# Optimization experiments

Hardware: AMD Instinct MI355X
Metric: run time of the kernel (lower is better)

## Reference

```python
import jax, jax.numpy as jnp
import numpy as np

NUM_HIDDEN = 128
NUM_IN = 256
NUM_HEADS = 4
B, T, N, K = 4, 32, 96, 30


def setup_inputs() -> dict:
    key = jax.random.key(0)
    ks = jax.random.split(key, 7)
    return {
        "h_V": jax.random.normal(ks[0], (B, T, N, NUM_HIDDEN), dtype=jnp.float32),
        "h_EV": jax.random.normal(ks[1], (B, T, N, K, NUM_IN), dtype=jnp.float32),
        "mask_attend": jax.random.randint(ks[2], (B, T, N, K), 0, 2, dtype=jnp.int32),
        "Wq": jax.random.normal(ks[3], (NUM_HIDDEN, NUM_HIDDEN), dtype=jnp.float32) / np.sqrt(NUM_HIDDEN),
        "Wk": jax.random.normal(ks[4], (NUM_IN, NUM_HIDDEN), dtype=jnp.float32) / np.sqrt(NUM_IN),
        "Wv": jax.random.normal(ks[5], (NUM_IN, NUM_HIDDEN), dtype=jnp.float32) / np.sqrt(NUM_IN),
        "Wo": jax.random.normal(ks[6], (NUM_HIDDEN, NUM_HIDDEN), dtype=jnp.float32) / np.sqrt(NUM_HIDDEN),
    }


def reference(h_V, h_EV, mask_attend, Wq, Wk, Wv, Wo):
    b, t, n, k = h_EV.shape[:4]
    h = NUM_HEADS
    d = NUM_HIDDEN // h
    # projections
    Q = (h_V @ Wq).reshape(b, t, n, h, d)            # [B,T,N,H,d]
    Kp = (h_EV @ Wk).reshape(b, t, n, k, h, d)       # [B,T,N,K,H,d]
    V = (h_EV @ Wv).reshape(b, t, n, k, h, d)        # [B,T,N,K,H,d]
    # per-node neighbor attention logits [B,T,N,H,K]
    logits = jnp.einsum('btnhd,btnkhd->btnhk', Q, Kp) / jnp.sqrt(jnp.float32(d))
    neg_inf = jnp.finfo(jnp.float32).min
    mask = mask_attend[:, :, :, None, :]             # [B,T,N,1,K] -> broadcast over heads
    logits = jnp.where(mask > 0, logits, neg_inf)
    attend = jax.nn.softmax(logits, axis=-1)
    attend = attend * mask.astype(jnp.float32)
    # combine values: [B,T,N,H,d]
    out = jnp.einsum('btnhk,btnkhd->btnhd', attend, V).reshape(b, t, n, NUM_HIDDEN)
    return out @ Wo
```

## Files before the change

kernel.cpp:

```cpp
#include <hip/hip_runtime.h>
#include <hip/hip_bf16.h>
#include <cfloat>
#include <math.h>

constexpr int SITES = 12288;
constexpr int KNB   = 30;
constexpr int CIN   = 256;
#define RSQRT_D 0.17677669529663689f

typedef short bf16x8 __attribute__((ext_vector_type(8)));
typedef float f32x4  __attribute__((ext_vector_type(4)));

__device__ inline unsigned short f2bs(float x) {
    __hip_bfloat16 b = __float2bfloat16(x);
    return *(unsigned short*)&b;
}
__device__ inline float bs2f(unsigned short u) {
    unsigned int v = (unsigned int)u << 16;
    float f;
    __builtin_memcpy(&f, &v, 4);
    return f;
}
__device__ inline unsigned int pack2(float a, float b) {
    return (unsigned int)f2bs(a) | ((unsigned int)f2bs(b) << 16);
}

__global__ __launch_bounds__(256) void precompute_w(
    const float* __restrict__ Wq, const float* __restrict__ Wk,
    const float* __restrict__ Wv, const float* __restrict__ Wo,
    unsigned short* __restrict__ Mt, unsigned short* __restrict__ W3t) {
    int gid = blockIdx.x * 256 + threadIdx.x;
    if (gid < 131072) {
        int p = gid >> 7;
        int i = gid & 127;
        int h = p >> 8;
        int c = p & 255;
        float s = 0.f;
        #pragma unroll
        for (int d = 0; d < 32; ++d)
            s += Wq[i * 128 + h * 32 + d] * Wk[c * 128 + h * 32 + d];
        Mt[gid] = f2bs(s);
    } else {
        int o = gid - 131072;
        int j = o >> 10;
        int rest = o & 1023;
        int h = rest >> 8;
        int c = rest & 255;
        float s = 0.f;
        #pragma unroll
        for (int d = 0; d < 32; ++d)
            s += Wv[c * 128 + h * 32 + d] * Wo[(h * 32 + d) * 128 + j];
        W3t[o] = f2bs(s);
    }
}

__global__ __launch_bounds__(256) void convert_hv(
    const float* __restrict__ hV, unsigned short* __restrict__ hVb) {
    int gid = blockIdx.x * 256 + threadIdx.x;
    const float4* src = (const float4*)hV;
    float4 a = src[gid * 2];
    float4 b = src[gid * 2 + 1];
    uint4 p;
    p.x = pack2(a.x, a.y);
    p.y = pack2(a.z, a.w);
    p.z = pack2(b.x, b.y);
    p.w = pack2(b.z, b.w);
    ((uint4*)hVb)[gid] = p;
}

template <bool OUT_BF16>
__global__ __launch_bounds__(256) void gemm_bt_bf16(
    const unsigned short* __restrict__ A, const unsigned short* __restrict__ Bt,
    void* __restrict__ C, int M, int N, int K) {
    constexpr int BM = 64, BN = 128, BK = 32, PAD = 8;
    constexpr int NT = BN / 16;
    __shared__ unsigned short As[BM][BK + PAD];
    __shared__ unsigned short Bs[BN][BK + PAD];
    const int tid  = threadIdx.x;
    const int wave = tid >> 6;
    const int lane = tid & 63;
    const int quad = lane >> 4;
    const int l16  = lane & 15;
    const int bm0 = blockIdx.x * BM;
    const int bn0 = blockIdx.y * BN;

    f32x4 acc[NT];
    #pragma unroll
    for (int j = 0; j < NT; ++j) acc[j] = (f32x4){0.f, 0.f, 0.f, 0.f};

    for (int kk = 0; kk < K; kk += BK) {
        {
            int row = tid >> 2, off = (tid & 3) * 8;
            *(uint4*)&As[row][off] =
                *(const uint4*)&A[(size_t)(bm0 + row) * K + kk + off];
        }
        #pragma unroll
        for (int i = 0; i < 2; ++i) {
            int c = tid * 2 + i;
            int row = c >> 2, off = (c & 3) * 8;
            *(uint4*)&Bs[row][off] =
                *(const uint4*)&Bt[(size_t)(bn0 + row) * K + kk + off];
        }
        __syncthreads();
        bf16x8 af = *(const bf16x8*)&As[wave * 16 + l16][quad * 8];
        #pragma unroll
        for (int j = 0; j < NT; ++j) {
            bf16x8 bf = *(const bf16x8*)&Bs[j * 16 + l16][quad * 8];
            acc[j] = __builtin_amdgcn_mfma_f32_16x16x32_bf16(af, bf, acc[j], 0, 0, 0);
        }
        __syncthreads();
    }
    int row0 = bm0 + wave * 16 + quad * 4;
    #pragma unroll
    for (int j = 0; j < NT; ++j) {
        int col = bn0 + j * 16 + l16;
        #pragma unroll
        for (int r = 0; r < 4; ++r) {
            if (OUT_BF16)
                ((unsigned short*)C)[(size_t)(row0 + r) * N + col] = f2bs(acc[j][r]);
            else
                ((float*)C)[(size_t)(row0 + r) * N + col] = acc[j][r];
        }
    }
}

__global__ __launch_bounds__(256) void attn_kernel(
    const float* __restrict__ hEV, const int* __restrict__ mask,
    const unsigned short* __restrict__ qt, unsigned short* __restrict__ evb) {
    __shared__ unsigned short evS[KNB * CIN];
    __shared__ float logitsL[4 * 32];
    __shared__ float attendL[4 * 32];
    __shared__ int   activeS[32];
    __shared__ int   naS;

    const int s = blockIdx.x;
    const int tid = threadIdx.x;
    const int lane = tid & 63;
    const int sub = tid & 15;

    if (tid < 64) {
        int mk = (tid < KNB) ? mask[(size_t)s * KNB + tid] : 0;
        unsigned long long bal = __ballot(mk > 0);
        if (tid == 0) naS = __popcll(bal);
        if (mk > 0) activeS[__popcll(bal & ((1ull << tid) - 1))] = tid;
    }

    float qf[4][16];
    {
        const uint4* q4 = (const uint4*)(qt + (size_t)s * 1024);
        #pragma unroll
        for (int h = 0; h < 4; ++h) {
            #pragma unroll
            for (int c = 0; c < 2; ++c) {
                uint4 u = q4[h * 32 + sub * 2 + c];
                qf[h][c * 8 + 0] = bs2f(u.x & 0xffff);
                qf[h][c * 8 + 1] = bs2f(u.x >> 16);
                qf[h][c * 8 + 2] = bs2f(u.y & 0xffff);
                qf[h][c * 8 + 3] = bs2f(u.y >> 16);
                qf[h][c * 8 + 4] = bs2f(u.z & 0xffff);
                qf[h][c * 8 + 5] = bs2f(u.z >> 16);
                qf[h][c * 8 + 6] = bs2f(u.w & 0xffff);
                qf[h][c * 8 + 7] = bs2f(u.w >> 16);
            }
        }
    }
    __syncthreads();
    const int na = naS;

    for (int r = tid >> 4; r < na; r += 16) {
        int k = activeS[r];
        const float4* row4 = (const float4*)(hEV + (size_t)s * (KNB * CIN) + (size_t)k * CIN);
        float vv[16];
        #pragma unroll
        for (int i = 0; i < 4; ++i)
            *(float4*)&vv[i * 4] = row4[sub * 4 + i];

        uint4 p0, p1;
        p0.x = pack2(vv[0], vv[1]);  p0.y = pack2(vv[2], vv[3]);
        p0.z = pack2(vv[4], vv[5]);  p0.w = pack2(vv[6], vv[7]);
        p1.x = pack2(vv[8], vv[9]);  p1.y = pack2(vv[10], vv[11]);
        p1.z = pack2(vv[12], vv[13]); p1.w = pack2(vv[14], vv[15]);
        *(uint4*)&evS[r * CIN + sub * 16]     = p0;
        *(uint4*)&evS[r * CIN + sub * 16 + 8] = p1;

        float l[4] = {0.f, 0.f, 0.f, 0.f};
        #pragma unroll
        for (int h = 0; h < 4; ++h)
            #pragma unroll
            for (int c = 0; c < 16; ++c)
                l[h] = fmaf(vv[c], qf[h][c], l[h]);

        #pragma unroll
        for (int m = 1; m < 16; m <<= 1) {
            #pragma unroll
            for (int h = 0; h < 4; ++h) l[h] += __shfl_xor(l[h], m, 64);
        }
        if (sub == 0) {
            #pragma unroll
            for (int h = 0; h < 4; ++h) logitsL[h * 32 + r] = l[h] * RSQRT_D;
        }
    }
    __syncthreads();

    {
        int h = tid >> 6;
        float lg = (lane < na) ? logitsL[h * 32 + lane] : -FLT_MAX;
        float mx = lg;
        #pragma unroll
        for (int m = 1; m < 64; m <<= 1) mx = fmaxf(mx, __shfl_xor(mx, m, 64));
        float e = (lane < na) ? __expf(lg - mx) : 0.f;
        float sm = e;
        #pragma unroll
        for (int m = 1; m < 64; m <<= 1) sm += __shfl_xor(sm, m, 64);
        if (lane < na) attendL[h * 32 + lane] = e / sm;
    }
    __syncthreads();

    float a0 = 0.f, a1 = 0.f, a2 = 0.f, a3 = 0.f;
    for (int r = 0; r < na; ++r) {
        float evv = bs2f(evS[r * CIN + tid]);
        a0 = fmaf(attendL[r], evv, a0);
        a1 = fmaf(attendL[32 + r], evv, a1);
        a2 = fmaf(attendL[64 + r], evv, a2);
        a3 = fmaf(attendL[96 + r], evv, a3);
    }
    size_t ob = (size_t)s * 1024 + tid;
    evb[ob]       = f2bs(a0);
    evb[ob + 256] = f2bs(a1);
    evb[ob + 512] = f2bs(a2);
    evb[ob + 768] = f2bs(a3);
}

extern "C" void kernel_launch(void* const* d_in, const int* in_sizes, int n_in,
                              void* d_out, int out_size, void* d_ws, size_t ws_size,
                              hipStream_t stream) {
    const float* hV   = (const float*)d_in[0];
    const float* hEV  = (const float*)d_in[1];
    const int*   mask = (const int*)d_in[2];
    const float* Wq   = (const float*)d_in[3];
    const float* Wk   = (const float*)d_in[4];
    const float* Wv   = (const float*)d_in[5];
    const float* Wo   = (const float*)d_in[6];
    float* out = (float*)d_out;

    unsigned short* ws = (unsigned short*)d_ws;
    unsigned short* Mt   = ws;
    unsigned short* W3t  = ws + 131072;
    unsigned short* hVb  = ws + 262144;
    unsigned short* qt   = ws + 262144 + 1572864;
    unsigned short* evb  = qt + (size_t)SITES * 1024;
    size_t need = ((size_t)262144 + 1572864 + 2 * (size_t)SITES * 1024) * 2;
    if (ws_size < need) return;

    precompute_w<<<dim3(1024), dim3(256), 0, stream>>>(Wq, Wk, Wv, Wo, Mt, W3t);
    convert_hv<<<dim3(768), dim3(256), 0, stream>>>(hV, hVb);

    gemm_bt_bf16<true><<<dim3(SITES / 64, 1024 / 128), dim3(256), 0, stream>>>(
        hVb, Mt, qt, SITES, 1024, 128);

    attn_kernel<<<dim3(SITES), dim3(256), 0, stream>>>(hEV, mask, qt, evb);

    gemm_bt_bf16<false><<<dim3(SITES / 64, 1), dim3(256), 0, stream>>>(
        evb, W3t, out, SITES, 128, 1024);
}
```

Baseline: 518.1 us.

## Fuse hV bf16 conversion into Q GEMM and widen attention row loads

The separate convert_hv kernel is removed, and the Q-projection GEMM now reads fp32 h_V directly and packs it to bf16 while staging into shared memory. The attention kernel stages q in shared memory through 128 threads and assigns each neighbor row to a 32-lane half-wave with 8 elements per lane, where before it used 16 lanes with 16 elements each. The precompute kernel uses float4 loads and a remapped W3t index so its Wo reads are coalesced. This saves one kernel launch and an intermediate buffer round trip, but the GEMM now re-reads the fp32 A tile once for each of its 8 column blocks and the logit reduction needs one extra shuffle level.

```diff
diff --git a/kernel.cpp b/kernel.cpp
--- a/kernel.cpp
+++ b/kernel.cpp
@@ -35,42 +35,34 @@
         int i = gid & 127;
         int h = p >> 8;
         int c = p & 255;
+        const float4* wq = (const float4*)(Wq + (size_t)i * 128 + h * 32);
+        const float4* wk = (const float4*)(Wk + (size_t)c * 128 + h * 32);
         float s = 0.f;
         #pragma unroll
-        for (int d = 0; d < 32; ++d)
-            s += Wq[i * 128 + h * 32 + d] * Wk[c * 128 + h * 32 + d];
+        for (int d = 0; d < 8; ++d) {
+            float4 a = wq[d], b = wk[d];
+            s += a.x * b.x; s += a.y * b.y; s += a.z * b.z; s += a.w * b.w;
+        }
         Mt[gid] = f2bs(s);
     } else {
         int o = gid - 131072;
-        int j = o >> 10;
-        int rest = o & 1023;
-        int h = rest >> 8;
-        int c = rest & 255;
+        int p = o >> 7;
+        int j = o & 127;
+        int h = p >> 8;
+        int c = p & 255;
+        const float* wv = Wv + (size_t)c * 128 + h * 32;
+        const float* wo = Wo + (size_t)(h * 32) * 128 + j;
         float s = 0.f;
         #pragma unroll
         for (int d = 0; d < 32; ++d)
-            s += Wv[c * 128 + h * 32 + d] * Wo[(h * 32 + d) * 128 + j];
-        W3t[o] = f2bs(s);
-    }
-}
-
-__global__ __launch_bounds__(256) void convert_hv(
-    const float* __restrict__ hV, unsigned short* __restrict__ hVb) {
-    int gid = blockIdx.x * 256 + threadIdx.x;
-    const float4* src = (const float4*)hV;
-    float4 a = src[gid * 2];
-    float4 b = src[gid * 2 + 1];
-    uint4 p;
-    p.x = pack2(a.x, a.y);
-    p.y = pack2(a.z, a.w);
-    p.z = pack2(b.x, b.y);
-    p.w = pack2(b.z, b.w);
-    ((uint4*)hVb)[gid] = p;
-}
-
-template <bool OUT_BF16>
+            s += wv[d] * wo[(size_t)d * 128];
+        W3t[(size_t)j * 1024 + p] = f2bs(s);
+    }
+}
+
+template <bool OUT_BF16, bool A_F32>
 __global__ __launch_bounds__(256) void gemm_bt_bf16(
-    const unsigned short* __restrict__ A, const unsigned short* __restrict__ Bt,
+    const void* __restrict__ Aptr, const unsigned short* __restrict__ Bt,
     void* __restrict__ C, int M, int N, int K) {
     constexpr int BM = 64, BN = 128, BK = 32, PAD = 8;
     constexpr int NT = BN / 16;
@@ -91,15 +83,26 @@
     for (int kk = 0; kk < K; kk += BK) {
         {
             int row = tid >> 2, off = (tid & 3) * 8;
-            *(uint4*)&As[row][off] =
-                *(const uint4*)&A[(size_t)(bm0 + row) * K + kk + off];
+            if (A_F32) {
+                const float* Af = (const float*)Aptr;
+                const float4* src = (const float4*)&Af[(size_t)(bm0 + row) * K + kk + off];
+                float4 a0 = src[0], a1 = src[1];
+                uint4 p;
+                p.x = pack2(a0.x, a0.y); p.y = pack2(a0.z, a0.w);
+                p.z = pack2(a1.x, a1.y); p.w = pack2(a1.z, a1.w);
+                *(uint4*)&As[row][off] = p;
+            } else {
+                const unsigned short* Ab = (const unsigned short*)Aptr;
+                *(uint4*)&As[row][off] =
+                    *(const uint4*)&Ab[(size_t)(bm0 + row) * K + kk + off];
+            }
         }
         #pragma unroll
         for (int i = 0; i < 2; ++i) {
-            int c = tid * 2 + i;
-            int row = c >> 2, off = (c & 3) * 8;
-            *(uint4*)&Bs[row][off] =
-                *(const uint4*)&Bt[(size_t)(bn0 + row) * K + kk + off];
+            int c2 = tid * 2 + i;
+            int brow = c2 >> 2, boff = (c2 & 3) * 8;
+            *(uint4*)&Bs[brow][boff] =
+                *(const uint4*)&Bt[(size_t)(bn0 + brow) * K + kk + boff];
         }
         __syncthreads();
         bf16x8 af = *(const bf16x8*)&As[wave * 16 + l16][quad * 8];
@@ -128,6 +131,7 @@
     const float* __restrict__ hEV, const int* __restrict__ mask,
     const unsigned short* __restrict__ qt, unsigned short* __restrict__ evb) {
     __shared__ unsigned short evS[KNB * CIN];
+    __shared__ float qS[1024];
     __shared__ float logitsL[4 * 32];
     __shared__ float attendL[4 * 32];
     __shared__ int   activeS[32];
@@ -136,66 +140,59 @@
     const int s = blockIdx.x;
     const int tid = threadIdx.x;
     const int lane = tid & 63;
-    const int sub = tid & 15;
+    const int wv = tid >> 6;
+    const int hw = lane >> 5;
+    const int sl = lane & 31;
 
     if (tid < 64) {
         int mk = (tid < KNB) ? mask[(size_t)s * KNB + tid] : 0;
         unsigned long long bal = __ballot(mk > 0);
         if (tid == 0) naS = __popcll(bal);
         if (mk > 0) activeS[__popcll(bal & ((1ull << tid) - 1))] = tid;
-    }
-
-    float qf[4][16];
-    {
-        const uint4* q4 = (const uint4*)(qt + (size_t)s * 1024);
+    } else if (tid < 192) {
+        int t2 = tid - 64;
+        uint4 u = ((const uint4*)(qt + (size_t)s * 1024))[t2];
+        float f[8];
+        f[0] = bs2f(u.x & 0xffff); f[1] = bs2f(u.x >> 16);
+        f[2] = bs2f(u.y & 0xffff); f[3] = bs2f(u.y >> 16);
+        f[4] = bs2f(u.z & 0xffff); f[5] = bs2f(u.z >> 16);
+        f[6] = bs2f(u.w & 0xffff); f[7] = bs2f(u.w >> 16);
+        *(float4*)&qS[t2 * 8]     = *(float4*)&f[0];
+        *(float4*)&qS[t2 * 8 + 4] = *(float4*)&f[4];
+    }
+    __syncthreads();
+
+    float qf[4][8];
+    #pragma unroll
+    for (int h = 0; h < 4; ++h) {
+        *(float4*)&qf[h][0] = *(const float4*)&qS[h * 256 + sl * 8];
+        *(float4*)&qf[h][4] = *(const float4*)&qS[h * 256 + sl * 8 + 4];
+    }
+    const int na = naS;
+
+    for (int r = wv * 2 + hw; r < na; r += 8) {
+        int k = activeS[r];
+        const float* row = hEV + (size_t)s * (KNB * CIN) + (size_t)k * CIN + sl * 8;
+        float4 v0 = *(const float4*)row;
+        float4 v1 = *(const float4*)(row + 4);
+
+        uint4 p;
+        p.x = pack2(v0.x, v0.y); p.y = pack2(v0.z, v0.w);
+        p.z = pack2(v1.x, v1.y); p.w = pack2(v1.z, v1.w);
+        *(uint4*)&evS[r * CIN + sl * 8] = p;
+
+        float l[4];
         #pragma unroll
         for (int h = 0; h < 4; ++h) {
-            #pragma unroll
-            for (int c = 0; c < 2; ++c) {
-                uint4 u = q4[h * 32 + sub * 2 + c];
-                qf[h][c * 8 + 0] = bs2f(u.x & 0xffff);
-                qf[h][c * 8 + 1] = bs2f(u.x >> 16);
-                qf[h][c * 8 + 2] = bs2f(u.y & 0xffff);
-                qf[h][c * 8 + 3] = bs2f(u.y >> 16);
-                qf[h][c * 8 + 4] = bs2f(u.z & 0xffff);
-                qf[h][c * 8 + 5] = bs2f(u.z >> 16);
-                qf[h][c * 8 + 6] = bs2f(u.w & 0xffff);
-                qf[h][c * 8 + 7] = bs2f(u.w >> 16);
-            }
-        }
-    }
-    __syncthreads();
-    const int na = naS;
-
-    for (int r = tid >> 4; r < na; r += 16) {
-        int k = activeS[r];
-        const float4* row4 = (const float4*)(hEV + (size_t)s * (KNB * CIN) + (size_t)k * CIN);
-        float vv[16];
-        #pragma unroll
-        for (int i = 0; i < 4; ++i)
-            *(float4*)&vv[i * 4] = row4[sub * 4 + i];
-
-        uint4 p0, p1;
-        p0.x = pack2(vv[0], vv[1]);  p0.y = pack2(vv[2], vv[3]);
-        p0.z = pack2(vv[4], vv[5]);  p0.w = pack2(vv[6], vv[7]);
-        p1.x = pack2(vv[8], vv[9]);  p1.y = pack2(vv[10], vv[11]);
-        p1.z = pack2(vv[12], vv[13]); p1.w = pack2(vv[14], vv[15]);
-        *(uint4*)&evS[r * CIN + sub * 16]     = p0;
-        *(uint4*)&evS[r * CIN + sub * 16 + 8] = p1;
-
-        float l[4] = {0.f, 0.f, 0.f, 0.f};
-        #pragma unroll
-        for (int h = 0; h < 4; ++h)
-            #pragma unroll
-            for (int c = 0; c < 16; ++c)
-                l[h] = fmaf(vv[c], qf[h][c], l[h]);
-
-        #pragma unroll
-        for (int m = 1; m < 16; m <<= 1) {
+            l[h] = v0.x * qf[h][0] + v0.y * qf[h][1] + v0.z * qf[h][2] + v0.w * qf[h][3]
+                 + v1.x * qf[h][4] + v1.y * qf[h][5] + v1.z * qf[h][6] + v1.w * qf[h][7];
+        }
+        #pragma unroll
+        for (int m = 1; m < 32; m <<= 1) {
             #pragma unroll
             for (int h = 0; h < 4; ++h) l[h] += __shfl_xor(l[h], m, 64);
         }
-        if (sub == 0) {
+        if (sl == 0) {
             #pragma unroll
             for (int h = 0; h < 4; ++h) logitsL[h * 32 + r] = l[h] * RSQRT_D;
         }
@@ -203,8 +200,7 @@
     __syncthreads();
 
     {
-        int h = tid >> 6;
-        float lg = (lane < na) ? logitsL[h * 32 + lane] : -FLT_MAX;
+        float lg = (lane < na) ? logitsL[wv * 32 + lane] : -FLT_MAX;
         float mx = lg;
         #pragma unroll
         for (int m = 1; m < 64; m <<= 1) mx = fmaxf(mx, __shfl_xor(mx, m, 64));
@@ -212,7 +208,7 @@
         float sm = e;
         #pragma unroll
         for (int m = 1; m < 64; m <<= 1) sm += __shfl_xor(sm, m, 64);
-        if (lane < na) attendL[h * 32 + lane] = e / sm;
+        if (lane < na) attendL[wv * 32 + lane] = e / sm;
     }
     __syncthreads();
 
@@ -246,20 +242,18 @@
     unsigned short* ws = (unsigned short*)d_ws;
     unsigned short* Mt   = ws;
     unsigned short* W3t  = ws + 131072;
-    unsigned short* hVb  = ws + 262144;
-    unsigned short* qt   = ws + 262144 + 1572864;
+    unsigned short* qt   = ws + 262144;
     unsigned short* evb  = qt + (size_t)SITES * 1024;
-    size_t need = ((size_t)262144 + 1572864 + 2 * (size_t)SITES * 1024) * 2;
+    size_t need = ((size_t)262144 + 2 * (size_t)SITES * 1024) * 2;
     if (ws_size < need) return;
 
     precompute_w<<<dim3(1024), dim3(256), 0, stream>>>(Wq, Wk, Wv, Wo, Mt, W3t);
-    convert_hv<<<dim3(768), dim3(256), 0, stream>>>(hV, hVb);
-
-    gemm_bt_bf16<true><<<dim3(SITES / 64, 1024 / 128), dim3(256), 0, stream>>>(
-        hVb, Mt, qt, SITES, 1024, 128);
+
+    gemm_bt_bf16<true, true><<<dim3(SITES / 64, 1024 / 128), dim3(256), 0, stream>>>(
+        hV, Mt, qt, SITES, 1024, 128);
 
     attn_kernel<<<dim3(SITES), dim3(256), 0, stream>>>(hEV, mask, qt, evb);
 
-    gemm_bt_bf16<false><<<dim3(SITES / 64, 1), dim3(256), 0, stream>>>(
+    gemm_bt_bf16<false, false><<<dim3(SITES / 64, 1), dim3(256), 0, stream>>>(
         evb, W3t, out, SITES, 128, 1024);
 }
```

Measured after the change: 511.9 us. No clear change (-1.2%).
